# Performance work log

Measured on AMD Instinct MI355X. Metric: run time of the kernel, lower is better.

Reference implementation:

```python
import jax, jax.numpy as jnp
import numpy as np

N_NODES = 100000
N_EDGES = 1600000
IN_DIM = 165
HIDDEN = 128
OUT_DIM = 2


def gcn_conv(x, W, b, src, dst, n_nodes):
    """PyG GCNConv: h = x @ W; add self-loops; sym-normalized scatter-add; + bias."""
    h = x @ W  # [N, F_out]
    loop = jnp.arange(n_nodes, dtype=src.dtype)
    src_f = jnp.concatenate([src, loop])  # [E + N]
    dst_f = jnp.concatenate([dst, loop])
    deg = jax.ops.segment_sum(jnp.ones(src_f.shape[0], dtype=h.dtype), dst_f,
                              num_segments=n_nodes)  # in-degree incl. self-loop
    dinv = jnp.where(deg > 0, jax.lax.rsqrt(deg), jnp.zeros_like(deg))
    norm = dinv[src_f] * dinv[dst_f]  # [E + N]
    msg = h[src_f] * norm[:, None]  # gather + scale, [E+N, F_out]
    out = jax.ops.segment_sum(msg, dst_f, num_segments=n_nodes)  # scatter-add
    return out + b


def setup_inputs() -> dict:
    key = jax.random.key(0)
    k_x, k_e, k_w1, k_b1, k_w2, k_b2 = jax.random.split(key, 6)
    x = jax.random.normal(k_x, (N_NODES, IN_DIM), dtype=jnp.float32)
    edge_index = jax.random.randint(k_e, (2, N_EDGES), 0, N_NODES, dtype=jnp.int64)
    # Glorot-like init for linear weights, zeros for bias (PyG defaults)
    W1 = jax.random.normal(k_w1, (IN_DIM, HIDDEN), dtype=jnp.float32) / np.sqrt(IN_DIM)
    b1 = jnp.zeros((HIDDEN,), dtype=jnp.float32)
    W2 = jax.random.normal(k_w2, (HIDDEN, OUT_DIM), dtype=jnp.float32) / np.sqrt(HIDDEN)
    b2 = jnp.zeros((OUT_DIM,), dtype=jnp.float32)
    return {"x": x, "edge_index": edge_index, "W1": W1, "b1": b1, "W2": W2, "b2": b2}


def reference(x, edge_index, W1, b1, W2, b2):
    src, dst = edge_index[0], edge_index[1]
    h = gcn_conv(x, W1, b1, src, dst, N_NODES)
    h = jax.nn.relu(h)
    # dropout: eval mode (training=False) -> identity
    out = gcn_conv(h, W2, b2, src, dst, N_NODES)
    return out
```

## Files before the change

kernel.cpp:

```cpp
#include <hip/hip_runtime.h>
#include <hip/hip_fp16.h>

#define N_NODES 100000
#define N_EDGES 1600000
#define IN_DIM  165
#define HIDDEN  128
#define OUT_DIM 2

#define NBKT 196
#define CHUNK 4096
#define NCHUNK ((N_EDGES + CHUNK - 1) / CHUNK)
#define PADCAP 10240
#define KPAD 176
#define GROWS 64
#define XSTRIDE 176

typedef _Float16 half8_t __attribute__((ext_vector_type(8)));
typedef _Float16 half4_t __attribute__((ext_vector_type(4)));
typedef float floatx4 __attribute__((ext_vector_type(4)));
typedef float floatx4_a4 __attribute__((ext_vector_type(4), aligned(4)));


__global__ __launch_bounds__(512) void k_part2(const int* __restrict__ src,
                                               const int* __restrict__ dst,
                                               int* __restrict__ bcnt,
                                               unsigned* __restrict__ arena) {
    __shared__ int hist[256];
    __shared__ int gbase[256];

    int t = threadIdx.x;
    int e0 = blockIdx.x * CHUNK;
    int nE = N_EDGES - e0; if (nE > CHUNK) nE = CHUNK;
    int n4 = nE >> 2;
    const int4* dst4 = (const int4*)(dst + e0);
    const int4* src4 = (const int4*)(src + e0);

    if (t < 256) hist[t] = 0;
    __syncthreads();

    for (int i = t; i < n4; i += 512) {
        int4 d = dst4[i];
        atomicAdd(&hist[d.x >> 9], 1);
        atomicAdd(&hist[d.y >> 9], 1);
        atomicAdd(&hist[d.z >> 9], 1);
        atomicAdd(&hist[d.w >> 9], 1);
    }
    __syncthreads();

    if (t < NBKT) gbase[t] = t * PADCAP + atomicAdd(&bcnt[t], hist[t]);
    if (t < 256) hist[t] = 0;
    __syncthreads();

    for (int i = t; i < n4; i += 512) {
        int4 d = dst4[i];
        int4 s = src4[i];
        #pragma unroll
        for (int j = 0; j < 4; j++) {
            int dd = (j == 0) ? d.x : (j == 1) ? d.y : (j == 2) ? d.z : d.w;
            int ss = (j == 0) ? s.x : (j == 1) ? s.y : (j == 2) ? s.z : s.w;
            int bk = dd >> 9;
            unsigned entry = (unsigned)ss | ((unsigned)(dd & 511) << 17);
            int idx = atomicAdd(&hist[bk], 1);
            arena[gbase[bk] + idx] = entry;
        }
    }
}


__global__ __launch_bounds__(1024) void k_sort4(const unsigned* __restrict__ arena,
                                                const int* __restrict__ bcnt,
                                                int* __restrict__ csr,
                                                int* __restrict__ rowstart,
                                                int* __restrict__ rowend,
                                                float* __restrict__ dinv) {
    __shared__ int cnt[512];
    __shared__ int cur[512];
    __shared__ int wsum[4];
    int b = blockIdx.x;
    int n0 = b << 9;
    int t = threadIdx.x;
    int lane = t & 63, wid = t >> 6;
    int total = bcnt[b];
    int abase = b * PADCAP;
    int dbase = b * PADCAP;
    int nt4 = total >> 2;
    const uint4* arena4 = (const uint4*)(arena + abase);

    if (t < 512) cnt[t] = 0;
    __syncthreads();
    for (int p = t; p < nt4; p += 1024) {
        uint4 e = arena4[p];
        atomicAdd(&cnt[e.x >> 17], 1);
        atomicAdd(&cnt[e.y >> 17], 1);
        atomicAdd(&cnt[e.z >> 17], 1);
        atomicAdd(&cnt[e.w >> 17], 1);
    }
    {
        int p = (nt4 << 2) + t;
        if (p < total) atomicAdd(&cnt[arena[abase + p] >> 17], 1);
    }
    __syncthreads();

    int c0 = 0, c1 = 0, s = 0, inc = 0;
    if (t < 256) {
        c0 = cnt[2 * t];
        c1 = cnt[2 * t + 1];
        s = c0 + c1;
        inc = s;
        #pragma unroll
        for (int off = 1; off < 64; off <<= 1) {
            int y = __shfl_up(inc, off);
            if (lane >= off) inc += y;
        }
        if (lane == 63) wsum[wid] = inc;
    }
    __syncthreads();
    if (t == 0) {
        int acc = 0;
        #pragma unroll
        for (int w = 0; w < 4; w++) { int tv = wsum[w]; wsum[w] = acc; acc += tv; }
    }
    __syncthreads();
    if (t < 256) {
        int base = dbase + wsum[wid] + (inc - s);
        cur[2 * t] = base;
        cur[2 * t + 1] = base + c0;
        int node0 = n0 + 2 * t;
        if (node0 < N_NODES) {
            rowstart[node0] = base;
            rowend[node0] = base + c0;
            dinv[node0] = rsqrtf((float)(c0 + 1));
        }
        if (node0 + 1 < N_NODES) {
            rowstart[node0 + 1] = base + c0;
            rowend[node0 + 1] = base + c0 + c1;
            dinv[node0 + 1] = rsqrtf((float)(c1 + 1));
        }
    }
    __syncthreads();

    for (int p = t; p < nt4; p += 1024) {
        uint4 e = arena4[p];
        #pragma unroll
        for (int j = 0; j < 4; j++) {
            unsigned entry = (j == 0) ? e.x : (j == 1) ? e.y : (j == 2) ? e.z : e.w;
            int local = (int)(entry >> 17);
            int sv = (int)(entry & 0x1FFFFu);
            int pos = atomicAdd(&cur[local], 1);
            csr[pos] = sv;
        }
    }
    {
        int p = (nt4 << 2) + t;
        if (p < total) {
            unsigned entry = arena[abase + p];
            int local = (int)(entry >> 17);
            int sv = (int)(entry & 0x1FFFFu);
            int pos = atomicAdd(&cur[local], 1);
            csr[pos] = sv;
        }
    }
}


__global__ void k_w1t(const float* __restrict__ W1, _Float16* __restrict__ w1t,
                      int* __restrict__ bcnt) {
    if (blockIdx.x == 0 && threadIdx.x < NBKT) bcnt[threadIdx.x] = 0;
    int idx = blockIdx.x * 256 + threadIdx.x;
    if (idx < HIDDEN * KPAD) {
        int c = idx / KPAD, k = idx - c * KPAD;
        float v = (k < IN_DIM) ? W1[k * HIDDEN + c] : 0.f;
        w1t[idx] = (_Float16)v;
    }
}


__global__ __launch_bounds__(256, 8) void k_gemm1(const float* __restrict__ x,
                                                  const _Float16* __restrict__ w1t,
                                                  const float* __restrict__ dinv,
                                                  _Float16* __restrict__ h1s) {
    __shared__ __align__(16) _Float16 xs[GROWS * XSTRIDE];
    int t = threadIdx.x;
    int wid = t >> 6, lane = t & 63;
    int row0 = blockIdx.x * GROWS;
    int nrows = N_NODES - row0; if (nrows > GROWS) nrows = GROWS;

    const float* xbase = x + (size_t)row0 * IN_DIM;
    constexpr int NG = XSTRIDE / 8;
    for (int idx = t; idx < GROWS * NG; idx += 256) {
        int r = idx / NG;
        if (r >= nrows) break;
        int g = idx - r * NG;
        int c0 = g * 8;
        half8_t h;
        if (c0 + 8 <= IN_DIM) {
            floatx4_a4 va = *(const floatx4_a4*)(xbase + r * IN_DIM + c0);
            floatx4_a4 vb = *(const floatx4_a4*)(xbase + r * IN_DIM + c0 + 4);
            #pragma unroll
            for (int j = 0; j < 4; j++) h[j] = (_Float16)va[j];
            #pragma unroll
            for (int j = 0; j < 4; j++) h[4 + j] = (_Float16)vb[j];
        } else {
            #pragma unroll
            for (int j = 0; j < 8; j++) {
                int c = c0 + j;
                h[j] = (c < IN_DIM) ? (_Float16)xbase[r * IN_DIM + c] : (_Float16)0.f;
            }
        }
        *(half8_t*)&xs[(r * XSTRIDE + c0) ^ ((r & 7) << 3)] = h;
    }
    __syncthreads();

    int mrow = wid * 16;
    if (mrow >= nrows) return;
    int m = lane & 15;
    int quad = lane >> 4;
    int rbase = (mrow + m) * XSTRIDE;
    int sm = (m & 7) << 3;
    int grow = row0 + mrow;

    floatx4 acc[8];
    #pragma unroll
    for (int i = 0; i < 8; i++) acc[i] = (floatx4)(0.f);

    #pragma unroll
    for (int kc = 0; kc < 5; kc++) {
        int kb = kc * 32 + quad * 8;
        half8_t a = *(const half8_t*)&xs[(rbase + kb) ^ sm];
        #pragma unroll
        for (int cb = 0; cb < 8; cb++) {
            int col = cb * 16 + m;
            half8_t bf = *(const half8_t*)&w1t[col * KPAD + kb];
            acc[cb] = __builtin_amdgcn_mfma_f32_16x16x32_f16(a, bf, acc[cb], 0, 0, 0);
        }
    }
    {
        int kb = 160 + quad * 4;
        half4_t a = *(const half4_t*)&xs[(rbase + kb) ^ sm];
        #pragma unroll
        for (int cb = 0; cb < 8; cb++) {
            int col = cb * 16 + m;
            half4_t bf = *(const half4_t*)&w1t[col * KPAD + kb];
            acc[cb] = __builtin_amdgcn_mfma_f32_16x16x16f16(a, bf, acc[cb], 0, 0, 0);
        }
    }
    float dv[4];
    #pragma unroll
    for (int r = 0; r < 4; r++) dv[r] = dinv[grow + quad * 4 + r];
    #pragma unroll
    for (int cb = 0; cb < 8; cb++) {
        #pragma unroll
        for (int r = 0; r < 4; r++) {
            h1s[(size_t)(grow + quad * 4 + r) * HIDDEN + cb * 16 + m] =
                (_Float16)(acc[cb][r] * dv[r]);
        }
    }
}


__global__ __launch_bounds__(256) void k_agg1(const _Float16* __restrict__ h1,
                                              const int* __restrict__ rowstart,
                                              const int* __restrict__ rowend,
                                              const int* __restrict__ csr,
                                              const float* __restrict__ dinv,
                                              const float* __restrict__ b1,
                                              const float* __restrict__ W2,
                                              float2* __restrict__ h2s,
                                              int nodeoff) {
    int wid = threadIdx.x >> 6, lane = threadIdx.x & 63;
    int el = lane & 15;
    int es = lane >> 4;
    int node = nodeoff + blockIdx.x * 4 + wid;

    float acc[8];
    {
        half8_t v = *(const half8_t*)(h1 + (size_t)node * HIDDEN + el * 8);
        #pragma unroll
        for (int j = 0; j < 8; j++) acc[j] = (es == 0) ? (float)v[j] : 0.f;
    }

    int p0 = rowstart[node], p1 = rowend[node];
    int p = p0 + es;
    for (; p + 4 < p1; p += 8) {
        int sA = csr[p];
        int sB = csr[p + 4];
        half8_t vA = *(const half8_t*)(h1 + (size_t)sA * HIDDEN + el * 8);
        half8_t vB = *(const half8_t*)(h1 + (size_t)sB * HIDDEN + el * 8);
        #pragma unroll
        for (int j = 0; j < 8; j++) acc[j] += (float)vA[j];
        #pragma unroll
        for (int j = 0; j < 8; j++) acc[j] += (float)vB[j];
    }
    if (p < p1) {
        int s = csr[p];
        half8_t v = *(const half8_t*)(h1 + (size_t)s * HIDDEN + el * 8);
        #pragma unroll
        for (int j = 0; j < 8; j++) acc[j] += (float)v[j];
    }

    #pragma unroll
    for (int j = 0; j < 8; j++) {
        acc[j] += __shfl_xor(acc[j], 16);
        acc[j] += __shfl_xor(acc[j], 32);
    }

    float di = dinv[node];
    float4 bb0 = ((const float4*)b1)[el * 2];
    float4 bb1 = ((const float4*)b1)[el * 2 + 1];
    float bv[8] = {bb0.x, bb0.y, bb0.z, bb0.w, bb1.x, bb1.y, bb1.z, bb1.w};
    float a0 = 0.f, a1 = 0.f;
    #pragma unroll
    for (int j = 0; j < 8; j++) {
        float z = fmaf(di, acc[j], bv[j]);
        float r = fmaxf(z, 0.f);
        float2 w = ((const float2*)W2)[el * 8 + j];
        a0 = fmaf(r, w.x, a0);
        a1 = fmaf(r, w.y, a1);
    }
    #pragma unroll
    for (int off = 8; off; off >>= 1) {
        a0 += __shfl_xor(a0, off);
        a1 += __shfl_xor(a1, off);
    }
    if (lane == 0) h2s[node] = make_float2(di * a0, di * a1);
}


__global__ __launch_bounds__(256) void k_agg2(const float2* __restrict__ h2s,
                                              const int* __restrict__ rowstart,
                                              const int* __restrict__ rowend,
                                              const int* __restrict__ csr,
                                              const float* __restrict__ dinv,
                                              const float* __restrict__ b2,
                                              float2* __restrict__ out) {
    int wid = threadIdx.x >> 6, lane = threadIdx.x & 63;
    int sub = lane >> 4, el = lane & 15;
    int node = blockIdx.x * 16 + wid * 4 + sub;
    int p0 = rowstart[node], p1 = rowend[node];
    float ax = 0.f, ay = 0.f;
    for (int p = p0 + el; p < p1; p += 16) {
        float2 g = h2s[csr[p]];
        ax += g.x;
        ay += g.y;
    }
    #pragma unroll
    for (int off = 8; off; off >>= 1) {
        ax += __shfl_xor(ax, off);
        ay += __shfl_xor(ay, off);
    }
    if (el == 0) {
        float2 self = h2s[node];
        float di = dinv[node];
        out[node] = make_float2(fmaf(di, self.x + ax, b2[0]),
                                fmaf(di, self.y + ay, b2[1]));
    }
}


extern "C" void kernel_launch(void* const* d_in, const int* in_sizes, int n_in,
                              void* d_out, int out_size, void* d_ws, size_t ws_size,
                              hipStream_t stream) {
    const float* x  = (const float*)d_in[0];
    const int*   ei = (const int*)d_in[1];
    const float* W1 = (const float*)d_in[2];
    const float* b1 = (const float*)d_in[3];
    const float* W2 = (const float*)d_in[4];
    const float* b2 = (const float*)d_in[5];
    float* out = (float*)d_out;

    const int* src = ei;
    const int* dst = ei + N_EDGES;

    char* ws = (char*)d_ws;
    size_t off = 0;
    auto alloc = [&](size_t bytes) -> void* {
        void* p = ws + off;
        off += (bytes + 255) & ~(size_t)255;
        return p;
    };
    _Float16* h1s      = (_Float16*)alloc((size_t)N_NODES * HIDDEN * 2);
    float*    dinv     = (float*)   alloc((size_t)N_NODES * 4);
    int*      rowstart = (int*)     alloc((size_t)N_NODES * 4);
    int*      rowend   = (int*)     alloc((size_t)N_NODES * 4);
    int*      bcnt     = (int*)     alloc((size_t)NBKT * 4);
    unsigned* arena    = (unsigned*)alloc((size_t)NBKT * PADCAP * 4);
    int*      csr      = (int*)     alloc((size_t)NBKT * PADCAP * 4);
    _Float16* w1t      = (_Float16*)alloc((size_t)HIDDEN * KPAD * 2);
    float2*   h2s      = (float2*)  alloc((size_t)N_NODES * 8);

    k_w1t<<<(HIDDEN * KPAD + 255) / 256, 256, 0, stream>>>(W1, w1t, bcnt);
    k_part2<<<NCHUNK, 512, 0, stream>>>(src, dst, bcnt, arena);
    k_sort4<<<NBKT, 1024, 0, stream>>>(arena, bcnt, csr, rowstart, rowend, dinv);
    k_gemm1<<<(N_NODES + GROWS - 1) / GROWS, 256, 0, stream>>>(x, w1t, dinv, h1s);
    k_agg1<<<N_NODES / 4, 256, 0, stream>>>(h1s, rowstart, rowend, csr, dinv, b1, W2, h2s, 0);
    k_agg2<<<N_NODES / 16, 256, 0, stream>>>(h2s, rowstart, rowend, csr, dinv, b2, (float2*)out);
}
```

Measured before the change: 247.7 us.

## Split layer-1 aggregation across two feature halves with partial-sum combine kernel

The layer-1 gather/aggregate kernel now processes each node in two blocks, each handling 64 of the 128 hidden features, so 8 edge streams per wave gather 128-byte half-rows instead of 4 streams gathering full rows. Each half computes a partial W2 projection, written to a partial buffer that reuses the arena, and a new small kernel sums the two halves. This is meant to increase memory-level parallelism per wave and improve cache locality of the gather working set. The cost is double the CSR index reads, an extra kernel launch, and an extra round trip through the partial buffer.

```diff
diff --git a/kernel.cpp b/kernel.cpp
--- a/kernel.cpp
+++ b/kernel.cpp
@@ -265,27 +265,29 @@
                                               const float* __restrict__ dinv,
                                               const float* __restrict__ b1,
                                               const float* __restrict__ W2,
-                                              float2* __restrict__ h2s,
-                                              int nodeoff) {
+                                              float2* __restrict__ h2part) {
     int wid = threadIdx.x >> 6, lane = threadIdx.x & 63;
-    int el = lane & 15;
-    int es = lane >> 4;
-    int node = nodeoff + blockIdx.x * 4 + wid;
+    int slice = blockIdx.x & 1;
+    int node = (blockIdx.x >> 1) * 4 + wid;
+    int el = lane & 7;
+    int es = lane >> 3;
+
+    const _Float16* hs = h1 + slice * 64;
 
     float acc[8];
     {
-        half8_t v = *(const half8_t*)(h1 + (size_t)node * HIDDEN + el * 8);
+        half8_t v = *(const half8_t*)(hs + (size_t)node * HIDDEN + el * 8);
         #pragma unroll
         for (int j = 0; j < 8; j++) acc[j] = (es == 0) ? (float)v[j] : 0.f;
     }
 
     int p0 = rowstart[node], p1 = rowend[node];
     int p = p0 + es;
-    for (; p + 4 < p1; p += 8) {
+    for (; p + 8 < p1; p += 16) {
         int sA = csr[p];
-        int sB = csr[p + 4];
-        half8_t vA = *(const half8_t*)(h1 + (size_t)sA * HIDDEN + el * 8);
-        half8_t vB = *(const half8_t*)(h1 + (size_t)sB * HIDDEN + el * 8);
+        int sB = csr[p + 8];
+        half8_t vA = *(const half8_t*)(hs + (size_t)sA * HIDDEN + el * 8);
+        half8_t vB = *(const half8_t*)(hs + (size_t)sB * HIDDEN + el * 8);
         #pragma unroll
         for (int j = 0; j < 8; j++) acc[j] += (float)vA[j];
         #pragma unroll
@@ -293,36 +295,49 @@
     }
     if (p < p1) {
         int s = csr[p];
-        half8_t v = *(const half8_t*)(h1 + (size_t)s * HIDDEN + el * 8);
+        half8_t v = *(const half8_t*)(hs + (size_t)s * HIDDEN + el * 8);
         #pragma unroll
         for (int j = 0; j < 8; j++) acc[j] += (float)v[j];
     }
 
     #pragma unroll
     for (int j = 0; j < 8; j++) {
+        acc[j] += __shfl_xor(acc[j], 8);
         acc[j] += __shfl_xor(acc[j], 16);
         acc[j] += __shfl_xor(acc[j], 32);
     }
 
     float di = dinv[node];
-    float4 bb0 = ((const float4*)b1)[el * 2];
-    float4 bb1 = ((const float4*)b1)[el * 2 + 1];
+    int f0 = slice * 64 + el * 8;
+    float4 bb0 = ((const float4*)b1)[f0 >> 2];
+    float4 bb1 = ((const float4*)b1)[(f0 >> 2) + 1];
     float bv[8] = {bb0.x, bb0.y, bb0.z, bb0.w, bb1.x, bb1.y, bb1.z, bb1.w};
     float a0 = 0.f, a1 = 0.f;
     #pragma unroll
     for (int j = 0; j < 8; j++) {
         float z = fmaf(di, acc[j], bv[j]);
         float r = fmaxf(z, 0.f);
-        float2 w = ((const float2*)W2)[el * 8 + j];
+        float2 w = ((const float2*)W2)[f0 + j];
         a0 = fmaf(r, w.x, a0);
         a1 = fmaf(r, w.y, a1);
     }
     #pragma unroll
-    for (int off = 8; off; off >>= 1) {
+    for (int off = 4; off; off >>= 1) {
         a0 += __shfl_xor(a0, off);
         a1 += __shfl_xor(a1, off);
     }
-    if (lane == 0) h2s[node] = make_float2(di * a0, di * a1);
+    if (lane == 0) h2part[(size_t)slice * N_NODES + node] = make_float2(di * a0, di * a1);
+}
+
+
+__global__ __launch_bounds__(256) void k_h2c(const float2* __restrict__ h2part,
+                                             float2* __restrict__ h2s) {
+    int n = blockIdx.x * 256 + threadIdx.x;
+    if (n < N_NODES) {
+        float2 a = h2part[n];
+        float2 b = h2part[(size_t)N_NODES + n];
+        h2s[n] = make_float2(a.x + b.x, a.y + b.y);
+    }
 }
 
 
@@ -387,11 +402,13 @@
     int*      csr      = (int*)     alloc((size_t)NBKT * PADCAP * 4);
     _Float16* w1t      = (_Float16*)alloc((size_t)HIDDEN * KPAD * 2);
     float2*   h2s      = (float2*)  alloc((size_t)N_NODES * 8);
+    float2*   h2part   = (float2*)arena;
 
     k_w1t<<<(HIDDEN * KPAD + 255) / 256, 256, 0, stream>>>(W1, w1t, bcnt);
     k_part2<<<NCHUNK, 512, 0, stream>>>(src, dst, bcnt, arena);
     k_sort4<<<NBKT, 1024, 0, stream>>>(arena, bcnt, csr, rowstart, rowend, dinv);
     k_gemm1<<<(N_NODES + GROWS - 1) / GROWS, 256, 0, stream>>>(x, w1t, dinv, h1s);
-    k_agg1<<<N_NODES / 4, 256, 0, stream>>>(h1s, rowstart, rowend, csr, dinv, b1, W2, h2s, 0);
+    k_agg1<<<(N_NODES / 4) * 2, 256, 0, stream>>>(h1s, rowstart, rowend, csr, dinv, b1, W2, h2part);
+    k_h2c<<<(N_NODES + 255) / 256, 256, 0, stream>>>(h2part, h2s);
     k_agg2<<<N_NODES / 16, 256, 0, stream>>>(h2s, rowstart, rowend, csr, dinv, b2, (float2*)out);
 }
```

Result: slower. 284.0 us (+14.6%).
